# Performance work log

Measured on AMD Instinct MI355X. Metric: run time of the kernel, lower is better.

The kernel has to match this reference:

```python
import jax, jax.numpy as jnp
import numpy as np

N_NODES = 100000
N_EDGES = 600000
N_GRAPHS = 128
IN_DIM = 4
HID = 32
HEADS1 = 4
NEG_SLOPE = 0.2


def _segment_softmax(e, seg, n):
    # e: [E, H], softmax over edges sharing the same destination node
    m = jax.ops.segment_max(e, seg, num_segments=n)
    ex = jnp.exp(e - m[seg])
    s = jax.ops.segment_sum(ex, seg, num_segments=n)
    return ex / s[seg]


def _gat_layer(x, src, dst, W, a_src, a_dst, b, heads, ch):
    # PyG GATConv: h = x W (per-head), alpha = softmax_dst(leaky_relu(a_s.h_src + a_d.h_dst))
    n = x.shape[0]
    h = (x @ W).reshape(n, heads, ch)                       # [N, H, C]
    al_s = jnp.einsum('nhc,hc->nh', h, a_src)               # [N, H]
    al_d = jnp.einsum('nhc,hc->nh', h, a_dst)
    e = jax.nn.leaky_relu(al_s[src] + al_d[dst], NEG_SLOPE)  # [E, H]
    alpha = _segment_softmax(e, dst, n)                      # [E, H]
    msg = h[src] * alpha[:, :, None]                         # [E, H, C]
    out = jax.ops.segment_sum(msg, dst, num_segments=n)     # [N, H, C]
    return out.reshape(n, heads * ch) + b


def setup_inputs() -> dict:
    key = jax.random.key(0)
    ks = jax.random.split(key, 16)
    s = 0.1
    return {
        'x': jax.random.normal(ks[0], (N_NODES, IN_DIM), jnp.float32),
        'edge_index': jax.random.randint(ks[1], (2, N_EDGES), 0, N_NODES, jnp.int64),
        'batch': jax.random.randint(ks[2], (N_NODES,), 0, N_GRAPHS, jnp.int64),
        'W1': jax.random.normal(ks[3], (IN_DIM, HEADS1 * HID), jnp.float32) * s,
        'a_s1': jax.random.normal(ks[4], (HEADS1, HID), jnp.float32) * s,
        'a_d1': jax.random.normal(ks[5], (HEADS1, HID), jnp.float32) * s,
        'b1': jnp.zeros((HEADS1 * HID,), jnp.float32),
        'W2': jax.random.normal(ks[6], (HEADS1 * HID, HID), jnp.float32) * s,
        'a_s2': jax.random.normal(ks[7], (1, HID), jnp.float32) * s,
        'a_d2': jax.random.normal(ks[8], (1, HID), jnp.float32) * s,
        'b2': jnp.zeros((HID,), jnp.float32),
        'Wc1': jax.random.normal(ks[9], (HID, 32), jnp.float32) * s,
        'bc1': jnp.zeros((32,), jnp.float32),
        'Wc2': jax.random.normal(ks[10], (32, 1), jnp.float32) * s,
        'bc2': jnp.zeros((1,), jnp.float32),
    }


def reference(x, edge_index, batch, W1, a_s1, a_d1, b1, W2, a_s2, a_d2, b2, Wc1, bc1, Wc2, bc2):
    n = x.shape[0]
    loops = jnp.arange(n, dtype=edge_index.dtype)
    src = jnp.concatenate([edge_index[0], loops])   # add_self_loops=True (PyG default)
    dst = jnp.concatenate([edge_index[1], loops])
    h = jax.nn.elu(_gat_layer(x, src, dst, W1, a_s1, a_d1, b1, HEADS1, HID))
    h = jax.nn.elu(_gat_layer(h, src, dst, W2, a_s2, a_d2, b2, 1, HID))
    # global_mean_pool
    sums = jax.ops.segment_sum(h, batch, num_segments=N_GRAPHS)
    cnt = jax.ops.segment_sum(jnp.ones((n, 1), h.dtype), batch, num_segments=N_GRAPHS)
    g = sums / jnp.maximum(cnt, 1.0)
    z = jax.nn.relu(g @ Wc1 + bc1)
    return jax.nn.sigmoid(z @ Wc2 + bc2)
```

## Files before the change

### kernel.cpp

```cpp
#include <hip/hip_runtime.h>
#include <hip/hip_fp16.h>
#include <float.h>

#define NEG 0.2f
#define NPART 16
#define PAD 32

typedef _Float16 half8 __attribute__((ext_vector_type(8)));
typedef float f32x4 __attribute__((ext_vector_type(4)));

__device__ __forceinline__ float lrelu(float x){ return x > 0.f ? x : NEG * x; }
__device__ __forceinline__ float elu1(float x){ return x > 0.f ? x : (__expf(x) - 1.f); }

__global__ void k_scat(const int* __restrict__ ei, const int* __restrict__ batch,
                       int* __restrict__ cur, int* __restrict__ csr_src,
                       float* __restrict__ gcnt, int N, int E){
  __shared__ float gc[128];
  int tid = threadIdx.x;
  bool doh = blockIdx.x < 256;
  if (doh && tid < 128) gc[tid] = 0.f;
  __syncthreads();
  int idx = blockIdx.x * 256 + tid;
  int gstr = gridDim.x * 256;
  for (int e = idx; e < E; e += gstr){
    int s = ei[e], d = ei[E + e];
    int pos = atomicAdd(cur + d, 1);
    if (pos < PAD) csr_src[(size_t)d * PAD + pos] = s;
  }
  if (doh){
    for (int n = idx; n < N; n += 256 * 256)
      atomicAdd(&gc[batch[n]], 1.f);
    __syncthreads();
    if (tid < 128 && gc[tid] != 0.f) atomicAdd(gcnt + tid, gc[tid]);
  }
}

__global__ void __launch_bounds__(256, 6)
k_layer1(const int* __restrict__ degp, const int* __restrict__ csr_src,
         const float* __restrict__ x, const float* __restrict__ W1,
         const float* __restrict__ as1, const float* __restrict__ ad1,
         const float* __restrict__ b1, const float* __restrict__ W2,
         const float* __restrict__ as2, const float* __restrict__ ad2,
         __half* __restrict__ h2h, float* __restrict__ als2,
         float* __restrict__ ald2, int N){
  __shared__ float PQ[2][16];
  __shared__ __align__(16) float xa[32][20];
  __shared__ __align__(16) _Float16 out1sh[32][136];
  __shared__ __align__(16) float h2sh[32][36];
  __shared__ float als_s[32], ald_s[32];
  int tid = threadIdx.x;
  const float4* x4 = (const float4*)x;

  int g1 = tid >> 3, l = tid & 7;
  int node1 = blockIdx.x * 32 + g1;
  int nd = node1 < N ? node1 : N - 1;
  int deg = degp[nd];
  size_t r0 = (size_t)nd * PAD;
  int s_pre = csr_src[r0 + l];
  int total = (node1 < N) ? deg + 1 : 0;
  int s0 = (l < deg) ? s_pre : nd;
  float4 xv0 = x4[s0];
  float4 xn = x4[nd];

  if (tid < 32){
    int which = tid >> 4, kh = tid & 15, k = kh >> 2, h = kh & 3;
    const float* a = which ? ad1 : as1;
    float s = 0.f;
    #pragma unroll 8
    for (int c = 0; c < 32; c++) s += W1[k*128 + h*32 + c] * a[h*32 + c];
    PQ[which][kh] = s;
  }
  __syncthreads();

  {
    float P[16], Q[16];
    #pragma unroll
    for (int i = 0; i < 16; i++){ P[i] = PQ[0][i]; Q[i] = PQ[1][i]; }
    float ald0 = xn.x*Q[0] + xn.y*Q[4] + xn.z*Q[8]  + xn.w*Q[12];
    float ald1_ = xn.x*Q[1] + xn.y*Q[5] + xn.z*Q[9]  + xn.w*Q[13];
    float ald2_ = xn.x*Q[2] + xn.y*Q[6] + xn.z*Q[10] + xn.w*Q[14];
    float ald3 = xn.x*Q[3] + xn.y*Q[7] + xn.z*Q[11] + xn.w*Q[15];
    float acc[16];
    #pragma unroll
    for (int i = 0; i < 16; i++) acc[i] = 0.f;
    float ss[4] = {0.f, 0.f, 0.f, 0.f};
    if (l < total){
      float4 xv = xv0;
      float a0 = xv.x*P[0] + xv.y*P[4] + xv.z*P[8]  + xv.w*P[12];
      float a1 = xv.x*P[1] + xv.y*P[5] + xv.z*P[9]  + xv.w*P[13];
      float a2 = xv.x*P[2] + xv.y*P[6] + xv.z*P[10] + xv.w*P[14];
      float a3 = xv.x*P[3] + xv.y*P[7] + xv.z*P[11] + xv.w*P[15];
      float e0 = __expf(lrelu(a0 + ald0));
      float e1 = __expf(lrelu(a1 + ald1_));
      float e2 = __expf(lrelu(a2 + ald2_));
      float e3 = __expf(lrelu(a3 + ald3));
      ss[0] += e0; ss[1] += e1; ss[2] += e2; ss[3] += e3;
      acc[0]  += e0*xv.x; acc[1]  += e0*xv.y; acc[2]  += e0*xv.z; acc[3]  += e0*xv.w;
      acc[4]  += e1*xv.x; acc[5]  += e1*xv.y; acc[6]  += e1*xv.z; acc[7]  += e1*xv.w;
      acc[8]  += e2*xv.x; acc[9]  += e2*xv.y; acc[10] += e2*xv.z; acc[11] += e2*xv.w;
      acc[12] += e3*xv.x; acc[13] += e3*xv.y; acc[14] += e3*xv.z; acc[15] += e3*xv.w;
    }
    for (int t = l + 8; t < total; t += 8){
      int s = (t < deg) ? csr_src[r0 + t] : nd;
      float4 xv = x4[s];
      float a0 = xv.x*P[0] + xv.y*P[4] + xv.z*P[8]  + xv.w*P[12];
      float a1 = xv.x*P[1] + xv.y*P[5] + xv.z*P[9]  + xv.w*P[13];
      float a2 = xv.x*P[2] + xv.y*P[6] + xv.z*P[10] + xv.w*P[14];
      float a3 = xv.x*P[3] + xv.y*P[7] + xv.z*P[11] + xv.w*P[15];
      float e0 = __expf(lrelu(a0 + ald0));
      float e1 = __expf(lrelu(a1 + ald1_));
      float e2 = __expf(lrelu(a2 + ald2_));
      float e3 = __expf(lrelu(a3 + ald3));
      ss[0] += e0; ss[1] += e1; ss[2] += e2; ss[3] += e3;
      acc[0]  += e0*xv.x; acc[1]  += e0*xv.y; acc[2]  += e0*xv.z; acc[3]  += e0*xv.w;
      acc[4]  += e1*xv.x; acc[5]  += e1*xv.y; acc[6]  += e1*xv.z; acc[7]  += e1*xv.w;
      acc[8]  += e2*xv.x; acc[9]  += e2*xv.y; acc[10] += e2*xv.z; acc[11] += e2*xv.w;
      acc[12] += e3*xv.x; acc[13] += e3*xv.y; acc[14] += e3*xv.z; acc[15] += e3*xv.w;
    }
    #pragma unroll
    for (int m = 4; m >= 1; m >>= 1){
      #pragma unroll
      for (int i = 0; i < 16; i++) acc[i] += __shfl_xor(acc[i], m, 8);
      #pragma unroll
      for (int i = 0; i < 4; i++)  ss[i]  += __shfl_xor(ss[i], m, 8);
    }
    if (l == 0){
      float* o = xa[g1];
      *(float4*)(o)      = make_float4(acc[0],  acc[1],  acc[2],  acc[3]);
      *(float4*)(o + 4)  = make_float4(acc[4],  acc[5],  acc[6],  acc[7]);
      *(float4*)(o + 8)  = make_float4(acc[8],  acc[9],  acc[10], acc[11]);
      *(float4*)(o + 12) = make_float4(acc[12], acc[13], acc[14], acc[15]);
      *(float4*)(o + 16) = make_float4(ss[0], ss[1], ss[2], ss[3]);
    }
  }
  __syncthreads();
  if (tid < 128) xa[tid >> 2][16 + (tid & 3)] = 1.f / xa[tid >> 2][16 + (tid & 3)];
  __builtin_amdgcn_sched_barrier(0);

  int wv = tid >> 6, lane = tid & 63;
  int wm = wv >> 1, wn = wv & 1;
  int lrow = lane & 15, lk8 = lane >> 4;
  half8 bf[4];
  #pragma unroll
  for (int t = 0; t < 4; t++){
    #pragma unroll
    for (int j = 0; j < 8; j++)
      bf[t][j] = (_Float16)W2[(t*32 + lk8*8 + j)*32 + wn*16 + lrow];
  }
  int c128 = ((wv & 1) << 6) | lane;
  int gbase = (wv >> 1) << 4;
  int hh = c128 >> 5;
  float w1c0 = W1[c128], w1c1 = W1[128 + c128];
  float w1c2 = W1[256 + c128], w1c3 = W1[384 + c128];
  float b1c = b1[c128];
  __syncthreads();

  #pragma unroll
  for (int i = 0; i < 16; i++){
    int g = gbase + i;
    const float* xg = xa[g];
    float4 xv = *(const float4*)(xg + hh*4);
    float rs = xg[16 + hh];
    float o = elu1((xv.x*w1c0 + xv.y*w1c1 + xv.z*w1c2 + xv.w*w1c3) * rs + b1c);
    out1sh[g][c128] = (_Float16)o;
  }
  __syncthreads();

  {
    f32x4 acc2 = {0.f, 0.f, 0.f, 0.f};
    #pragma unroll
    for (int t = 0; t < 4; t++){
      half8 af = *(const half8*)(&out1sh[wm*16 + lrow][t*32 + lk8*8]);
      acc2 = __builtin_amdgcn_mfma_f32_16x16x32_f16(af, bf[t], acc2, 0, 0, 0);
    }
    #pragma unroll
    for (int i = 0; i < 4; i++)
      h2sh[wm*16 + lk8*4 + i][wn*16 + lrow] = acc2[i];
  }
  __syncthreads();

  {
    int g = tid >> 3, q = tid & 7;
    int node = blockIdx.x * 32 + g;
    float4 hv = *(const float4*)(&h2sh[g][q*4]);
    if (node < N){
      __half2 pa = __floats2half2_rn(hv.x, hv.y);
      __half2 pb = __floats2half2_rn(hv.z, hv.w);
      __half2* dst = (__half2*)(h2h + (size_t)node*32 + q*4);
      dst[0] = pa; dst[1] = pb;
    }
    float4 sa = *(const float4*)(as2 + q*4);
    float4 da = *(const float4*)(ad2 + q*4);
    float ps = hv.x*sa.x + hv.y*sa.y + hv.z*sa.z + hv.w*sa.w;
    float pd = hv.x*da.x + hv.y*da.y + hv.z*da.z + hv.w*da.w;
    #pragma unroll
    for (int m = 4; m >= 1; m >>= 1){
      ps += __shfl_xor(ps, m, 8);
      pd += __shfl_xor(pd, m, 8);
    }
    if (q == 0){ als_s[g] = ps; ald_s[g] = pd; }
  }
  __syncthreads();
  if (tid < 32){
    int node = blockIdx.x * 32 + tid;
    if (node < N){ als2[node] = als_s[tid]; ald2[node] = ald_s[tid]; }
  }
}

__global__ void __launch_bounds__(256)
k_gat2(const int* __restrict__ degp, const int* __restrict__ csr_src,
       const __half* __restrict__ h2h, const float* __restrict__ als2,
       const float* __restrict__ ald2, const float* __restrict__ b2,
       const int* __restrict__ batch, float* __restrict__ gsum_part, int N){
  int tid = threadIdx.x;
  int node = blockIdx.x * 8 + (tid >> 5);
  if (node >= N) return;
  int lane = tid & 31;
  int sub = lane >> 3;
  int c4 = lane & 7;
  int deg = degp[node];
  size_t r0 = (size_t)node * PAD;
  int total = deg + 1;
  float ald = ald2[node];

  float ssum = 0.f;
  float f0 = 0.f, f1 = 0.f, f2 = 0.f, f3 = 0.f;
  for (int base = 0; base < total; base += 32){
    int t = base + lane;
    int s = (t < deg) ? csr_src[r0 + t] : node;
    float ex = (t < total) ? __expf(lrelu(als2[s] + ald)) : 0.f;
    ssum += ex;
    int lim = min(32, total - base);
    for (int jj = 0; jj < lim; jj += 8){
      int ja = jj + sub, jb = jj + 4 + sub;
      float ea = __shfl(ex, ja, 32); int sa = __shfl(s, ja, 32);
      float eb = __shfl(ex, jb, 32); int sb = __shfl(s, jb, 32);
      union { float2 f; __half2 h[2]; } ua, ub;
      ua.f = *(const float2*)(h2h + (size_t)sa*32 + (c4 << 2));
      ub.f = *(const float2*)(h2h + (size_t)sb*32 + (c4 << 2));
      float2 va0 = __half22float2(ua.h[0]), va1 = __half22float2(ua.h[1]);
      float2 vb0 = __half22float2(ub.h[0]), vb1 = __half22float2(ub.h[1]);
      f0 += ea*va0.x + eb*vb0.x;
      f1 += ea*va0.y + eb*vb0.y;
      f2 += ea*va1.x + eb*vb1.x;
      f3 += ea*va1.y + eb*vb1.y;
    }
  }
  f0 += __shfl_xor(f0, 8, 32);  f0 += __shfl_xor(f0, 16, 32);
  f1 += __shfl_xor(f1, 8, 32);  f1 += __shfl_xor(f1, 16, 32);
  f2 += __shfl_xor(f2, 8, 32);  f2 += __shfl_xor(f2, 16, 32);
  f3 += __shfl_xor(f3, 8, 32);  f3 += __shfl_xor(f3, 16, 32);
  #pragma unroll
  for (int m = 16; m >= 1; m >>= 1) ssum += __shfl_xor(ssum, m, 32);
  float fc = (sub & 1) ? ((sub & 2) ? f3 : f1) : ((sub & 2) ? f2 : f0);
  int ch = (c4 << 2) + sub;
  float v = elu1(fc / ssum + b2[ch]);
  int b = batch[node];
  atomicAdd(gsum_part + ((blockIdx.x & (NPART-1)) << 12) + b*32 + ch, v);
}

__global__ void k_head(const float* __restrict__ gsum_part, const float* __restrict__ gcnt,
                       const float* __restrict__ Wc1, const float* __restrict__ bc1,
                       const float* __restrict__ Wc2, const float* __restrict__ bc2,
                       float* __restrict__ out){
  int g = blockIdx.x, tid = threadIdx.x;
  __shared__ float gl[32];
  if (tid < 32){
    float s = 0.f;
    #pragma unroll
    for (int p = 0; p < NPART; p++) s += gsum_part[(p << 12) + g*32 + tid];
    float cnt = gcnt[g];
    cnt = cnt > 1.f ? cnt : 1.f;
    gl[tid] = s / cnt;
  }
  __syncthreads();
  if (tid < 32){
    float z = bc1[tid];
    #pragma unroll 8
    for (int c2 = 0; c2 < 32; c2++) z += gl[c2] * Wc1[c2*32 + tid];
    z = z > 0.f ? z : 0.f;
    float r = z * Wc2[tid];
    #pragma unroll
    for (int m = 16; m >= 1; m >>= 1) r += __shfl_xor(r, m, 32);
    if (tid == 0) out[g] = 1.f / (1.f + expf(-(r + bc2[0])));
  }
}

extern "C" void kernel_launch(void* const* d_in, const int* in_sizes, int n_in,
                              void* d_out, int out_size, void* d_ws, size_t ws_size,
                              hipStream_t stream){
  const float* x   = (const float*)d_in[0];
  const int*   ei  = (const int*)d_in[1];
  const int*   bat = (const int*)d_in[2];
  const float* W1  = (const float*)d_in[3];
  const float* as1 = (const float*)d_in[4];
  const float* ad1 = (const float*)d_in[5];
  const float* b1  = (const float*)d_in[6];
  const float* W2  = (const float*)d_in[7];
  const float* as2 = (const float*)d_in[8];
  const float* ad2 = (const float*)d_in[9];
  const float* b2  = (const float*)d_in[10];
  const float* Wc1 = (const float*)d_in[11];
  const float* bc1 = (const float*)d_in[12];
  const float* Wc2 = (const float*)d_in[13];
  const float* bc2 = (const float*)d_in[14];
  float* out = (float*)d_out;

  const int N = in_sizes[2];
  const int E = in_sizes[1] / 2;

  float* ws = (float*)d_ws;
  size_t off = 0;
  int* cur    = (int*)ws;           off += (size_t)N;
  float* gsum_part = ws + off;      off += (size_t)NPART * 4096;
  float* gcnt = ws + off;           off += 128;
  const size_t zero_elems = off;
  __half* h2h = (__half*)(ws + off); off += (size_t)N * 16;
  float* als2 = ws + off;           off += (size_t)N;
  float* ald2 = ws + off;           off += (size_t)N;
  int* csr_src= (int*)(ws + off);   off += (size_t)N * PAD;

  hipMemsetAsync(d_ws, 0, zero_elems * sizeof(float), stream);

  k_scat<<<(E + 255) / 256, 256, 0, stream>>>(ei, bat, cur, csr_src, gcnt, N, E);

  k_layer1<<<(N + 31) / 32, 256, 0, stream>>>(cur, csr_src, x, W1, as1, ad1, b1,
                                              W2, as2, ad2, h2h, als2, ald2, N);

  k_gat2<<<(N + 7) / 8, 256, 0, stream>>>(cur, csr_src, h2h, als2, ald2, b2,
                                          bat, gsum_part, N);

  k_head<<<128, 64, 0, stream>>>(gsum_part, gcnt, Wc1, bc1, Wc2, bc2, out);
}
```

Baseline: 170.4 us.

## Process layer-2 aggregation with 8 lanes per node instead of 32

The layer-2 GAT aggregation kernel now gives each destination node 8 lanes instead of 32, so a block covers 32 nodes. Each lane owns 4 output channels and loops over neighbors in chunks of 8, broadcasting source indices and weights by shuffle. This removes the cross-subgroup reduction and wasted lanes for low-degree nodes, since average degree is about 7. In exchange each lane issues four atomics and the gather loop runs serially per neighbor, always doing 8 iterations per chunk even when fewer edges remain.

```diff
diff --git a/kernel.cpp b/kernel.cpp
--- a/kernel.cpp
+++ b/kernel.cpp
@@ -213,50 +213,42 @@
        const float* __restrict__ ald2, const float* __restrict__ b2,
        const int* __restrict__ batch, float* __restrict__ gsum_part, int N){
   int tid = threadIdx.x;
-  int node = blockIdx.x * 8 + (tid >> 5);
+  int node = blockIdx.x * 32 + (tid >> 3);
   if (node >= N) return;
-  int lane = tid & 31;
-  int sub = lane >> 3;
-  int c4 = lane & 7;
+  int l = tid & 7;
   int deg = degp[node];
   size_t r0 = (size_t)node * PAD;
   int total = deg + 1;
   float ald = ald2[node];
+  float4 b2v = *(const float4*)(b2 + (l << 2));
 
   float ssum = 0.f;
   float f0 = 0.f, f1 = 0.f, f2 = 0.f, f3 = 0.f;
-  for (int base = 0; base < total; base += 32){
-    int t = base + lane;
+  for (int base = 0; base < total; base += 8){
+    int t = base + l;
     int s = (t < deg) ? csr_src[r0 + t] : node;
     float ex = (t < total) ? __expf(lrelu(als2[s] + ald)) : 0.f;
     ssum += ex;
-    int lim = min(32, total - base);
-    for (int jj = 0; jj < lim; jj += 8){
-      int ja = jj + sub, jb = jj + 4 + sub;
-      float ea = __shfl(ex, ja, 32); int sa = __shfl(s, ja, 32);
-      float eb = __shfl(ex, jb, 32); int sb = __shfl(s, jb, 32);
-      union { float2 f; __half2 h[2]; } ua, ub;
-      ua.f = *(const float2*)(h2h + (size_t)sa*32 + (c4 << 2));
-      ub.f = *(const float2*)(h2h + (size_t)sb*32 + (c4 << 2));
-      float2 va0 = __half22float2(ua.h[0]), va1 = __half22float2(ua.h[1]);
-      float2 vb0 = __half22float2(ub.h[0]), vb1 = __half22float2(ub.h[1]);
-      f0 += ea*va0.x + eb*vb0.x;
-      f1 += ea*va0.y + eb*vb0.y;
-      f2 += ea*va1.x + eb*vb1.x;
-      f3 += ea*va1.y + eb*vb1.y;
-    }
-  }
-  f0 += __shfl_xor(f0, 8, 32);  f0 += __shfl_xor(f0, 16, 32);
-  f1 += __shfl_xor(f1, 8, 32);  f1 += __shfl_xor(f1, 16, 32);
-  f2 += __shfl_xor(f2, 8, 32);  f2 += __shfl_xor(f2, 16, 32);
-  f3 += __shfl_xor(f3, 8, 32);  f3 += __shfl_xor(f3, 16, 32);
-  #pragma unroll
-  for (int m = 16; m >= 1; m >>= 1) ssum += __shfl_xor(ssum, m, 32);
-  float fc = (sub & 1) ? ((sub & 2) ? f3 : f1) : ((sub & 2) ? f2 : f0);
-  int ch = (c4 << 2) + sub;
-  float v = elu1(fc / ssum + b2[ch]);
+    #pragma unroll
+    for (int j = 0; j < 8; j++){
+      float ej = __shfl(ex, j, 8);
+      int   sj = __shfl(s,  j, 8);
+      union { float2 f; __half2 h[2]; } u;
+      u.f = *(const float2*)(h2h + (size_t)sj*32 + (l << 2));
+      float2 v0 = __half22float2(u.h[0]), v1 = __half22float2(u.h[1]);
+      f0 += ej*v0.x; f1 += ej*v0.y; f2 += ej*v1.x; f3 += ej*v1.y;
+    }
+  }
+  ssum += __shfl_xor(ssum, 1, 8);
+  ssum += __shfl_xor(ssum, 2, 8);
+  ssum += __shfl_xor(ssum, 4, 8);
+  float rs = 1.f / ssum;
   int b = batch[node];
-  atomicAdd(gsum_part + ((blockIdx.x & (NPART-1)) << 12) + b*32 + ch, v);
+  float* gp = gsum_part + ((blockIdx.x & (NPART-1)) << 12) + b*32 + (l << 2);
+  atomicAdd(gp + 0, elu1(f0*rs + b2v.x));
+  atomicAdd(gp + 1, elu1(f1*rs + b2v.y));
+  atomicAdd(gp + 2, elu1(f2*rs + b2v.z));
+  atomicAdd(gp + 3, elu1(f3*rs + b2v.w));
 }
 
 __global__ void k_head(const float* __restrict__ gsum_part, const float* __restrict__ gcnt,
@@ -327,8 +319,8 @@
   k_layer1<<<(N + 31) / 32, 256, 0, stream>>>(cur, csr_src, x, W1, as1, ad1, b1,
                                               W2, as2, ad2, h2h, als2, ald2, N);
 
-  k_gat2<<<(N + 7) / 8, 256, 0, stream>>>(cur, csr_src, h2h, als2, ald2, b2,
-                                          bat, gsum_part, N);
+  k_gat2<<<(N + 31) / 32, 256, 0, stream>>>(cur, csr_src, h2h, als2, ald2, b2,
+                                            bat, gsum_part, N);
 
   k_head<<<128, 64, 0, stream>>>(gsum_part, gcnt, Wc1, bc1, Wc2, bc2, out);
 }
```

Measured after the change: 199.9 us. 17.3% more time.
